# Kernel optimization log

Hardware: AMD Instinct MI355X
Metric: run time of the kernel (lower is better)

Reference implementation:

```python
import jax, jax.numpy as jnp
import numpy as np

B, S, C, H = 2, 4096, 1024, 16
DH = C // H  # 64
# diffusers: attn.scale = dim_head ** -0.5; code divides scores by scale**0.5
SCALE = 1.0 / (float(DH) ** -0.25)  # == DH ** 0.25


def setup_inputs() -> dict:
    key = jax.random.key(0)
    ks = jax.random.split(key, 6)
    w = 0.02
    return {
        "hidden_states": jax.random.normal(ks[0], (B, S, C), jnp.float32),
        "Wq": jax.random.normal(ks[1], (C, C), jnp.float32) * w,
        "Wk": jax.random.normal(ks[2], (C, C), jnp.float32) * w,
        "Wv": jax.random.normal(ks[3], (C, C), jnp.float32) * w,
        "Wo": jax.random.normal(ks[4], (C, C), jnp.float32) * w,
        "bo": jnp.zeros((C,), jnp.float32),
        # token sizes >= 1 (number of patches each token represents)
        "token_sizes": jax.random.randint(ks[5], (B, S), 1, 17, jnp.int32),
    }


def _split_heads(x):
    # [B, S, C] -> [B, H, S, DH]
    return x.reshape(B, S, H, DH).transpose(0, 2, 1, 3)


def reference(hidden_states, Wq, Wk, Wv, Wo, bo, token_sizes):
    q = _split_heads(hidden_states @ Wq)  # [B,H,S,DH]
    k = _split_heads(hidden_states @ Wk)
    v = _split_heads(hidden_states @ Wv)
    # QK^T with diffusers-style scaling: scores / attn.scale**0.5 == scores * DH**0.25
    scores = jnp.einsum("bhqd,bhkd->bhqk", q, k) * SCALE  # [B,H,S,S]
    # additive log(token_size) bias over keys (self-attention path)
    log_sizes = jnp.log(token_sizes.astype(jnp.float32))  # [B,S]
    scores = scores + log_sizes[:, None, None, :]
    probs = jax.nn.softmax(scores, axis=-1)
    out = jnp.einsum("bhqk,bhkd->bhqd", probs, v)  # [B,H,S,DH]
    out = out.transpose(0, 2, 1, 3).reshape(B, S, C)  # merge heads
    return out @ Wo + bo  # to_out[0] linear; to_out[1] dropout is identity
```

## Files before the change

### kernel.cpp

```cpp
#include <hip/hip_runtime.h>


typedef unsigned short u16;
typedef unsigned int u32;
typedef _Float16 f16x8 __attribute__((ext_vector_type(8)));
typedef float f32x4 __attribute__((ext_vector_type(4)));
typedef short short4v __attribute__((ext_vector_type(4)));

constexpr int SEQ = 4096, CDIM = 1024, NH = 16, DHE = 64;
constexpr float SCALE2 = 2.8284271247461903f * 1.4426950408889634f;

template <int N> struct IC { static constexpr int v = N; };

union Frag { f16x8 v; short4v h[2]; };

__device__ __forceinline__ u16 f2h(float f) {
  union { _Float16 h; u16 u; } x;
  x.h = (_Float16)f;
  return x.u;
}

__device__ __forceinline__ u32 pkrtz(float a, float b) {
  u32 r;
  asm("v_cvt_pkrtz_f16_f32 %0, %1, %2" : "=v"(r) : "v"(a), "v"(b));
  return r;
}

__device__ __forceinline__ short4v pk4(const f32x4& v) {
  union { u32 w[2]; short4v s; } u;
  u.w[0] = pkrtz(v[0], v[1]);
  u.w[1] = pkrtz(v[2], v[3]);
  return u.s;
}

__device__ __forceinline__ float exp2fast(float x) {
  float r;
  asm("v_exp_f32 %0, %1" : "=v"(r) : "v"(x));
  return r;
}

__device__ __forceinline__ f32x4 mfma16(const Frag& a, const Frag& b, f32x4 c) {
  return __builtin_amdgcn_mfma_f32_16x16x32_f16(a.v, b.v, c, 0, 0, 0);
}

__device__ __forceinline__ void gl16(const void* g, void* l) {
  __builtin_amdgcn_global_load_lds(
      (const __attribute__((address_space(1))) u32*)g,
      (__attribute__((address_space(3))) u32*)l, 16, 0, 0);
}


__global__ __launch_bounds__(256) void prep_kernel(
    const float* __restrict__ x, u16* __restrict__ xout,
    const float* __restrict__ Wq, const float* __restrict__ Wk,
    const float* __restrict__ Wv, const float* __restrict__ Wo,
    u16* __restrict__ dq, u16* __restrict__ dk,
    u16* __restrict__ dv, u16* __restrict__ dow,
    const int* __restrict__ ts, u16* __restrict__ tsout) {
  __shared__ float tile[64][65];
  const int bidx = blockIdx.x;
  if (bidx < 4096) {
    size_t i = ((size_t)bidx * 256 + threadIdx.x) * 8;
    float4 a = *(const float4*)(x + i);
    float4 b = *(const float4*)(x + i + 4);
    uint4 o;
    o.x = (u32)f2h(a.x) | ((u32)f2h(a.y) << 16);
    o.y = (u32)f2h(a.z) | ((u32)f2h(a.w) << 16);
    o.z = (u32)f2h(b.x) | ((u32)f2h(b.y) << 16);
    o.w = (u32)f2h(b.z) | ((u32)f2h(b.w) << 16);
    *(uint4*)(xout + i) = o;
  } else if (bidx < 5120) {
    const int idx = bidx - 4096;
    const int z = idx >> 8, rem = idx & 255;
    const float* src;
    u16* dst;
    switch (z) {
      case 0: src = Wq; dst = dq; break;
      case 1: src = Wk; dst = dk; break;
      case 2: src = Wv; dst = dv; break;
      default: src = Wo; dst = dow; break;
    }
    const int r0 = (rem >> 4) * 64, c0 = (rem & 15) * 64;
    const int tx = threadIdx.x & 63, ty = threadIdx.x >> 6;
#pragma unroll
    for (int i = 0; i < 16; ++i) {
      const int row = i * 4 + ty;
      tile[row][tx] = src[(size_t)(r0 + row) * 1024 + c0 + tx];
    }
    __syncthreads();
#pragma unroll
    for (int i = 0; i < 16; ++i) {
      const int row = i * 4 + ty;
      dst[(size_t)(c0 + row) * 1024 + r0 + tx] = f2h(tile[tx][row]);
    }
  } else {
    const int i = (bidx - 5120) * 256 + threadIdx.x;
    tsout[i] = f2h((float)ts[i]);
  }
}


template <int EPI, int NBX>
__global__ __launch_bounds__(256) void gemm_f16(const u16* __restrict__ A,
                                                const u16* __restrict__ Bt,
                                                void* __restrict__ Out,
                                                const float* __restrict__ bias,
                                                const int* __restrict__ ts) {
  __shared__ __align__(16) short Alds[2][128 * 32];
  __shared__ __align__(16) short Blds[2][128 * 32];
  const int t = threadIdx.x;
  const int fid = blockIdx.x + NBX * blockIdx.y;
  constexpr int CPX = NBX * 64 / 8;
  const int wid = (fid & 7) * CPX + (fid >> 3);
  const int bnb = wid % NBX;
  const int bm = wid / NBX;
  const int lane = t & 63, wv = t >> 6;
  const int wm = wv >> 1, wn = wv & 1;
  const int l16 = lane & 15, lq = lane >> 4;

  f32x4 acc[4][4];
  f32x4 z = {0.f, 0.f, 0.f, 0.f};
#pragma unroll
  for (int i = 0; i < 4; ++i)
#pragma unroll
    for (int j = 0; j < 4; ++j) acc[i][j] = z;

  const int srow = t >> 2;
  const int schunk = (t & 3) ^ ((t >> 3) & 3);
  const u16* Ag = A + (size_t)(bm * 128 + srow) * 1024 + schunk * 8;
  const u16* Bg = Bt + (size_t)(bnb * 128 + srow) * 1024 + schunk * 8;
  const int dof = (t >> 6) * 512;

  auto stage = [&](int kb, int bufi) {
    const int k0 = kb * 32;
    short* Ad = &Alds[bufi][0] + dof;
    short* Bd = &Blds[bufi][0] + dof;
    gl16(Ag + k0, Ad);
    gl16(Ag + 64 * 1024 + k0, Ad + 2048);
    gl16(Bg + k0, Bd);
    gl16(Bg + 64 * 1024 + k0, Bd + 2048);
  };

  const int m2 = (l16 >> 1) & 3;
  const int o0 = (((lq >> 1) ^ m2) * 8) + (lq & 1) * 4;
  const int o1 = ((((lq >> 1) | 2) ^ m2) * 8) + (lq & 1) * 4;

  stage(0, 0);
  __syncthreads();

  for (int kb = 0; kb < 32; ++kb) {
    if (kb < 31) stage(kb + 1, (kb + 1) & 1);
    const short* Ab = &Alds[kb & 1][0];
    const short* Bb = &Blds[kb & 1][0];

    Frag af[4], bf[4];
#pragma unroll
    for (int am = 0; am < 4; ++am) {
      const short* p = Ab + (wm * 64 + am * 16 + l16) * 32;
      af[am].h[0] = *(const short4v*)(p + o0);
      af[am].h[1] = *(const short4v*)(p + o1);
    }
#pragma unroll
    for (int bn = 0; bn < 4; ++bn) {
      const short* p = Bb + (wn * 64 + bn * 16 + l16) * 32;
      bf[bn].h[0] = *(const short4v*)(p + o0);
      bf[bn].h[1] = *(const short4v*)(p + o1);
    }
#pragma unroll
    for (int am = 0; am < 4; ++am)
#pragma unroll
      for (int bn = 0; bn < 4; ++bn) acc[am][bn] = mfma16(af[am], bf[bn], acc[am][bn]);
    __syncthreads();
  }

#pragma unroll
  for (int am = 0; am < 4; ++am) {
#pragma unroll
    for (int bn = 0; bn < 4; ++bn) {
#pragma unroll
      for (int r = 0; r < 4; ++r) {
        const int m = bm * 128 + wm * 64 + am * 16 + lq * 4 + r;
        const int n = bnb * 128 + wn * 64 + bn * 16 + l16;
        float vsum = acc[am][bn][r];
        if (EPI == 0) {
          const int which = n >> 10;
          const int nn = n & 1023;
          const int h = nn >> 6, d = nn & 63;
          const int b = m >> 12, s = m & 4095;
          const int bhh = b * NH + h;
          size_t addr;
          if (which == 2) {
            vsum *= (float)ts[b * SEQ + s];
            addr = (size_t)2 * 8388608 + ((size_t)bhh * DHE + d) * SEQ + s;
          } else {
            if (which == 0) vsum *= SCALE2;
            addr = (size_t)which * 8388608 + ((size_t)bhh * SEQ + s) * DHE + d;
          }
          ((u16*)Out)[addr] = f2h(vsum);
        } else {
          ((float*)Out)[(size_t)m * 1024 + n] = vsum + bias[n];
        }
      }
    }
  }
}


__global__ __launch_bounds__(256, 2) void attn_kernel(const u16* __restrict__ Q,
                                                      const u16* __restrict__ K,
                                                      const u16* __restrict__ Vt,
                                                      const u16* __restrict__ ts16,
                                                      u16* __restrict__ Out) {
  __shared__ __align__(16) short Klds[2][64][72];
  __shared__ __align__(16) short Vtlds[2][64][72];

  const int t = threadIdx.x;
  const int bid = (blockIdx.x & 7) * 64 + (blockIdx.x >> 3);
  const int bh = bid >> 4;
  const int qb = bid & 15;
  const int lane = t & 63, wv = t >> 6;
  const int l16 = lane & 15, lq = lane >> 4;
  const int b = bh >> 4, h = bh & 15;

  Frag qf[4][2];
#pragma unroll
  for (int qh = 0; qh < 4; ++qh) {
    const int qrow = qb * 256 + wv * 64 + qh * 16 + l16;
    const u16* qp = Q + ((size_t)bh * SEQ + qrow) * DHE;
#pragma unroll
    for (int f = 0; f < 2; ++f) {
      qf[qh][f].h[0] = *(const short4v*)(qp + f * 32 + lq * 4);
      qf[qh][f].h[1] = *(const short4v*)(qp + f * 32 + lq * 4 + 16);
    }
  }

  float mrow[4] = {0.f, 0.f, 0.f, 0.f};
  f32x4 lsum[4];
  f32x4 oacc[4][4];
  f32x4 z = {0.f, 0.f, 0.f, 0.f};
#pragma unroll
  for (int qh = 0; qh < 4; ++qh) {
    lsum[qh] = z;
#pragma unroll
    for (int d = 0; d < 4; ++d) oacc[qh][d] = z;
  }

  const int a7 = t & 7, sd = a7 * 8, skey = t >> 3;
  const int vd = t >> 2, voct = (t & 3) * 8;
  const int vsw = ((vd >> 3) & 7) << 3;

  const u16* Kbase = K + (size_t)bh * SEQ * DHE;
  const u16* Vtbase = Vt + ((size_t)bh * DHE + vd) * SEQ;
  const u16* tsb = ts16 + b * SEQ;

  uint4 kv0 = *(const uint4*)(Kbase + (size_t)skey * DHE + sd);
  uint4 kv1 = *(const uint4*)(Kbase + (size_t)(skey + 32) * DHE + sd);
  uint4 vv0 = *(const uint4*)(Vtbase + voct);
  uint4 vv1 = *(const uint4*)(Vtbase + voct + 32);

  Frag tsfr[2];
  Frag paf[4][2];
  f32x4 scA[4], scB[4];

  for (int kt = 0; kt < 64; ++kt) {
    short (*Kb)[72] = Klds[kt & 1];
    short (*Vb)[72] = Vtlds[kt & 1];
    *(uint4*)&Kb[skey][sd] = kv0;
    *(uint4*)&Kb[skey + 32][sd] = kv1;
    *(uint4*)&Vb[vd][voct ^ vsw] = vv0;
    *(uint4*)&Vb[vd][(voct + 32) ^ vsw] = vv1;

    __syncthreads();

    if (kt < 63) {
      const u16* Kn = Kbase + (size_t)(kt + 1) * 64 * DHE + (size_t)skey * DHE + sd;
      kv0 = *(const uint4*)(Kn);
      kv1 = *(const uint4*)(Kn + 32 * DHE);
      const u16* Vn = Vtbase + (kt + 1) * 64 + voct;
      vv0 = *(const uint4*)(Vn);
      vv1 = *(const uint4*)(Vn + 32);
    }

    {
      const u16* tst = tsb + kt * 64;
#pragma unroll
      for (int kh = 0; kh < 2; ++kh) {
        tsfr[kh].h[0] = *(const short4v*)(tst + kh * 32 + lq * 4);
        tsfr[kh].h[1] = *(const short4v*)(tst + kh * 32 + lq * 4 + 16);
      }
    }

    Frag kfr[4][2];
#pragma unroll
    for (int k2 = 0; k2 < 4; ++k2) {
#pragma unroll
      for (int f = 0; f < 2; ++f) {
        const short* p = &Kb[k2 * 16 + l16][f * 32 + lq * 4];
        kfr[k2][f].h[0] = *(const short4v*)p;
        kfr[k2][f].h[1] = *(const short4v*)(p + 16);
      }
    }

    auto qkq = [&](auto qc, f32x4 (&sc)[4]) {
      constexpr int qh = decltype(qc)::v;
      const float nm = -mrow[qh];
      f32x4 seed = {nm, nm, nm, nm};
#pragma unroll
      for (int k2 = 0; k2 < 4; ++k2) {
        f32x4 a = mfma16(kfr[k2][0], qf[qh][0], seed);
        sc[k2] = mfma16(kfr[k2][1], qf[qh][1], a);
      }
    };

    auto smq = [&](auto qc, f32x4 (&sc)[4]) {
      constexpr int qh = decltype(qc)::v;
      float hm[4];
#pragma unroll
      for (int k2 = 0; k2 < 4; ++k2) {
        const f32x4 s = sc[k2];
        hm[k2] = fmaxf(fmaxf(s[0], s[1]), fmaxf(s[2], s[3]));
      }
      float mx = fmaxf(fmaxf(hm[0], hm[1]), fmaxf(hm[2], hm[3]));
      mx = fmaxf(mx, __shfl_xor(mx, 16));
      mx = fmaxf(mx, __shfl_xor(mx, 32));
      if (__any(mx > 8.f)) {
        const float sh = fmaxf(mx, 0.f);
        const float al = exp2fast(-sh);
        mrow[qh] += sh;
        f32x4 alv;
#pragma unroll
        for (int r = 0; r < 4; ++r) alv[r] = __shfl(al, lq * 4 + r, 16);
#pragma unroll
        for (int dd = 0; dd < 4; ++dd) oacc[qh][dd] *= alv;
        lsum[qh] *= alv;
#pragma unroll
        for (int k2 = 0; k2 < 4; ++k2) sc[k2] -= sh;
      }
#pragma unroll
      for (int k2 = 0; k2 < 4; ++k2) {
        f32x4 s = sc[k2];
#pragma unroll
        for (int r = 0; r < 4; ++r) s[r] = exp2fast(s[r]);
        sc[k2] = s;
      }
      paf[qh][0].h[0] = pk4(sc[0]); paf[qh][0].h[1] = pk4(sc[1]);
      paf[qh][1].h[0] = pk4(sc[2]); paf[qh][1].h[1] = pk4(sc[3]);
      lsum[qh] = mfma16(paf[qh][0], tsfr[0], lsum[qh]);
      lsum[qh] = mfma16(paf[qh][1], tsfr[1], lsum[qh]);
    };

    qkq(IC<0>{}, scA);
    qkq(IC<1>{}, scB);
    smq(IC<0>{}, scA);
    qkq(IC<2>{}, scA);
    smq(IC<1>{}, scB);
    qkq(IC<3>{}, scB);
    smq(IC<2>{}, scA);
    smq(IC<3>{}, scB);

    __builtin_amdgcn_s_setprio(1);
#pragma unroll
    for (int dd = 0; dd < 4; ++dd) {
      const int vrow = dd * 16 + l16;
      const int e = ((vrow >> 3) & 7) << 3;
#pragma unroll
      for (int kh = 0; kh < 2; ++kh) {
        Frag vb;
        vb.h[0] = *(const short4v*)&Vb[vrow][(kh * 32 + lq * 4) ^ e];
        vb.h[1] = *(const short4v*)&Vb[vrow][(kh * 32 + 16 + lq * 4) ^ e];
#pragma unroll
        for (int qh = 0; qh < 4; ++qh)
          oacc[qh][dd] = mfma16(paf[qh][kh], vb, oacc[qh][dd]);
      }
    }
    __builtin_amdgcn_s_setprio(0);
  }

#pragma unroll
  for (int qh = 0; qh < 4; ++qh) {
    f32x4 linv;
#pragma unroll
    for (int r = 0; r < 4; ++r) linv[r] = 1.f / lsum[qh][r];
#pragma unroll
    for (int dd = 0; dd < 4; ++dd) {
#pragma unroll
      for (int r = 0; r < 4; ++r) {
        const int row = qb * 256 + wv * 64 + qh * 16 + lq * 4 + r;
        const float v = oacc[qh][dd][r] * linv[r];
        Out[((size_t)b * SEQ + row) * CDIM + h * DHE + dd * 16 + l16] = f2h(v);
      }
    }
  }
}


extern "C" void kernel_launch(void* const* d_in, const int* in_sizes, int n_in,
                              void* d_out, int out_size, void* d_ws, size_t ws_size,
                              hipStream_t stream) {
  const float* hs = (const float*)d_in[0];
  const float* Wq = (const float*)d_in[1];
  const float* Wk = (const float*)d_in[2];
  const float* Wv = (const float*)d_in[3];
  const float* Wo = (const float*)d_in[4];
  const float* bo = (const float*)d_in[5];
  const int* ts = (const int*)d_in[6];
  float* out = (float*)d_out;

  char* ws = (char*)d_ws;
  u16* xf = (u16*)(ws);
  u16* wtq = (u16*)(ws + 16777216);
  u16* wtk = (u16*)(ws + 18874368);
  u16* wtv = (u16*)(ws + 20971520);
  u16* wto = (u16*)(ws + 23068672);
  u16* qbuf = (u16*)(ws + 25165824);
  u16* kbuf = (u16*)(ws + 41943040);
  u16* vtbuf = (u16*)(ws + 58720256);
  u16* ts16 = (u16*)(ws + 75497472);

  prep_kernel<<<5152, 256, 0, stream>>>(hs, xf, Wq, Wk, Wv, Wo,
                                        wtq, wtk, wtv, wto, ts, ts16);

  gemm_f16<0, 24><<<dim3(24, 64), 256, 0, stream>>>(xf, wtq, (void*)qbuf, nullptr, ts);

  attn_kernel<<<512, 256, 0, stream>>>(qbuf, kbuf, vtbuf, ts16, xf);

  gemm_f16<1, 8><<<dim3(8, 64), 256, 0, stream>>>(xf, wto, (void*)out, bo, nullptr);

  (void)in_sizes; (void)n_in; (void)out_size; (void)ws_size;
}
```

Before: 321.2 us.

## Halve attention block to 128 threads and double grid to 1024 blocks

The attention kernel now uses 2 waves per block (128 query rows) instead of 4, launching 1024 blocks rather than 512. The K/V staging into shared memory is reworked so each thread loads four 16-byte chunks of one row half, keeping full 64-key tile coverage with fewer threads. The aim is more blocks than the 256 CUs for better load balance and occupancy. In exchange, each K/V tile is reloaded by twice as many blocks, doubling global traffic for keys and values, and each thread issues more loads per tile.

New measurement: 490.0 us. 1.53x slower.

```diff
diff --git a/kernel.cpp b/kernel.cpp
--- a/kernel.cpp
+++ b/kernel.cpp
@@ -206,7 +206,7 @@
 }
 
 
-__global__ __launch_bounds__(256, 2) void attn_kernel(const u16* __restrict__ Q,
+__global__ __launch_bounds__(128, 2) void attn_kernel(const u16* __restrict__ Q,
                                                       const u16* __restrict__ K,
                                                       const u16* __restrict__ Vt,
                                                       const u16* __restrict__ ts16,
@@ -215,9 +215,9 @@
   __shared__ __align__(16) short Vtlds[2][64][72];
 
   const int t = threadIdx.x;
-  const int bid = (blockIdx.x & 7) * 64 + (blockIdx.x >> 3);
-  const int bh = bid >> 4;
-  const int qb = bid & 15;
+  const int bid = (blockIdx.x & 7) * 128 + (blockIdx.x >> 3);
+  const int bh = bid >> 5;
+  const int qb = bid & 31;
   const int lane = t & 63, wv = t >> 6;
   const int l16 = lane & 15, lq = lane >> 4;
   const int b = bh >> 4, h = bh & 15;
@@ -225,7 +225,7 @@
   Frag qf[4][2];
 #pragma unroll
   for (int qh = 0; qh < 4; ++qh) {
-    const int qrow = qb * 256 + wv * 64 + qh * 16 + l16;
+    const int qrow = qb * 128 + wv * 64 + qh * 16 + l16;
     const u16* qp = Q + ((size_t)bh * SEQ + qrow) * DHE;
 #pragma unroll
     for (int f = 0; f < 2; ++f) {
@@ -245,18 +245,24 @@
     for (int d = 0; d < 4; ++d) oacc[qh][d] = z;
   }
 
-  const int a7 = t & 7, sd = a7 * 8, skey = t >> 3;
-  const int vd = t >> 2, voct = (t & 3) * 8;
-  const int vsw = ((vd >> 3) & 7) << 3;
+  const int srow = t >> 1;
+  const int shalf = (t & 1) * 32;
+  const int vsw = ((srow >> 3) & 7) << 3;
 
   const u16* Kbase = K + (size_t)bh * SEQ * DHE;
-  const u16* Vtbase = Vt + ((size_t)bh * DHE + vd) * SEQ;
+  const u16* Vtbase = Vt + ((size_t)bh * DHE + srow) * SEQ;
   const u16* tsb = ts16 + b * SEQ;
 
-  uint4 kv0 = *(const uint4*)(Kbase + (size_t)skey * DHE + sd);
-  uint4 kv1 = *(const uint4*)(Kbase + (size_t)(skey + 32) * DHE + sd);
-  uint4 vv0 = *(const uint4*)(Vtbase + voct);
-  uint4 vv1 = *(const uint4*)(Vtbase + voct + 32);
+  uint4 kv[4], vv[4];
+  {
+    const u16* K0 = Kbase + (size_t)srow * DHE + shalf;
+    const u16* V0 = Vtbase + shalf;
+#pragma unroll
+    for (int j = 0; j < 4; ++j) {
+      kv[j] = *(const uint4*)(K0 + j * 8);
+      vv[j] = *(const uint4*)(V0 + j * 8);
+    }
+  }
 
   Frag tsfr[2];
   Frag paf[4][2];
@@ -265,20 +271,22 @@
   for (int kt = 0; kt < 64; ++kt) {
     short (*Kb)[72] = Klds[kt & 1];
     short (*Vb)[72] = Vtlds[kt & 1];
-    *(uint4*)&Kb[skey][sd] = kv0;
-    *(uint4*)&Kb[skey + 32][sd] = kv1;
-    *(uint4*)&Vb[vd][voct ^ vsw] = vv0;
-    *(uint4*)&Vb[vd][(voct + 32) ^ vsw] = vv1;
+#pragma unroll
+    for (int j = 0; j < 4; ++j) {
+      *(uint4*)&Kb[srow][shalf + j * 8] = kv[j];
+      *(uint4*)&Vb[srow][(shalf + j * 8) ^ vsw] = vv[j];
+    }
 
     __syncthreads();
 
     if (kt < 63) {
-      const u16* Kn = Kbase + (size_t)(kt + 1) * 64 * DHE + (size_t)skey * DHE + sd;
-      kv0 = *(const uint4*)(Kn);
-      kv1 = *(const uint4*)(Kn + 32 * DHE);
-      const u16* Vn = Vtbase + (kt + 1) * 64 + voct;
-      vv0 = *(const uint4*)(Vn);
-      vv1 = *(const uint4*)(Vn + 32);
+      const u16* Kn = Kbase + (size_t)(kt + 1) * 64 * DHE + (size_t)srow * DHE + shalf;
+      const u16* Vn = Vtbase + (kt + 1) * 64 + shalf;
+#pragma unroll
+      for (int j = 0; j < 4; ++j) {
+        kv[j] = *(const uint4*)(Kn + j * 8);
+        vv[j] = *(const uint4*)(Vn + j * 8);
+      }
     }
 
     {
@@ -385,7 +393,7 @@
     for (int dd = 0; dd < 4; ++dd) {
 #pragma unroll
       for (int r = 0; r < 4; ++r) {
-        const int row = qb * 256 + wv * 64 + qh * 16 + lq * 4 + r;
+        const int row = qb * 128 + wv * 64 + qh * 16 + lq * 4 + r;
         const float v = oacc[qh][dd][r] * linv[r];
         Out[((size_t)b * SEQ + row) * CDIM + h * DHE + dd * 16 + l16] = f2h(v);
       }
@@ -422,7 +430,7 @@
 
   gemm_f16<0, 24><<<dim3(24, 64), 256, 0, stream>>>(xf, wtq, (void*)qbuf, nullptr, ts);
 
-  attn_kernel<<<512, 256, 0, stream>>>(qbuf, kbuf, vtbuf, ts16, xf);
+  attn_kernel<<<1024, 128, 0, stream>>>(qbuf, kbuf, vtbuf, ts16, xf);
 
   gemm_f16<1, 8><<<dim3(8, 64), 256, 0, stream>>>(xf, wto, (void*)out, bo, nullptr);
 
```
